# Optimization experiments

Hardware: AMD Instinct MI355X
Metric: run time of the kernel (lower is better)

The kernel has to match this reference:

```python
import jax, jax.numpy as jnp
import numpy as np

DIM = 768
HEADS = 12
HIDDEN = 3072  # dim * mlp_ratio
EPS = 1e-5


def layernorm(x, g, b):
    mu = jnp.mean(x, axis=-1, keepdims=True)
    var = jnp.var(x, axis=-1, keepdims=True)
    return (x - mu) * jax.lax.rsqrt(var + EPS) * g + b


def setup_inputs() -> dict:
    key = jax.random.key(0)
    ks = jax.random.split(key, 10)
    s = 0.02
    return {
        "x": jax.random.normal(ks[0], (4, 1024, DIM), jnp.float32),
        "attention_mask": jax.random.randint(ks[1], (4, 1024), 0, 2, jnp.int32),
        "ln1_g": jnp.ones((DIM,), jnp.float32),
        "ln1_b": jnp.zeros((DIM,), jnp.float32),
        "ln2_g": jnp.ones((DIM,), jnp.float32),
        "ln2_b": jnp.zeros((DIM,), jnp.float32),
        "w_qkv": jax.random.normal(ks[2], (DIM, 3 * DIM), jnp.float32) * s,
        "b_qkv": jnp.zeros((3 * DIM,), jnp.float32),
        "w_proj": jax.random.normal(ks[3], (DIM, DIM), jnp.float32) * s,
        "b_proj": jnp.zeros((DIM,), jnp.float32),
        "w_fc1": jax.random.normal(ks[4], (DIM, HIDDEN), jnp.float32) * s,
        "b_fc1": jnp.zeros((HIDDEN,), jnp.float32),
        "w_fc2": jax.random.normal(ks[5], (HIDDEN, DIM), jnp.float32) * s,
        "b_fc2": jnp.zeros((DIM,), jnp.float32),
    }


def reference(x, attention_mask, ln1_g, ln1_b, ln2_g, ln2_b,
              w_qkv, b_qkv, w_proj, b_proj, w_fc1, b_fc1, w_fc2, b_fc2):
    B, N, C = x.shape
    hd = C // HEADS
    scale = hd ** -0.5

    # --- attention branch ---
    h = layernorm(x, ln1_g, ln1_b)
    qkv = (h @ w_qkv + b_qkv).reshape(B, N, 3, HEADS, hd)
    q, k, v = qkv[:, :, 0], qkv[:, :, 1], qkv[:, :, 2]  # [B,N,H,hd]
    attn = jnp.einsum('bnhd,bmhd->bhnm', q, k) * scale
    mask_bias = jnp.where(attention_mask == 0, -10000.0, 0.0)[:, None, None, :]
    attn = jax.nn.softmax(attn + mask_bias, axis=-1)
    o = jnp.einsum('bhnm,bmhd->bnhd', attn, v).reshape(B, N, C)
    x = x + (o @ w_proj + b_proj)

    # --- MLP branch ---
    h = layernorm(x, ln2_g, ln2_b)
    h = jax.nn.gelu(h @ w_fc1 + b_fc1, approximate=False)
    x = x + (h @ w_fc2 + b_fc2)
    return x
```

## Files before the change

### kernel.cpp

```cpp
#include <hip/hip_runtime.h>

#define DIM 768
#define NTOK 4096
#define HID 3072

typedef __attribute__((ext_vector_type(8))) short bf16x8;
typedef __attribute__((ext_vector_type(4))) float f32x4;

__device__ inline unsigned short f2bf(float f){
  unsigned u = __float_as_uint(f);
  u += 0x7fff + ((u >> 16) & 1);
  return (unsigned short)(u >> 16);
}
__device__ inline unsigned cvt_pk_bf16(float a, float b){
  unsigned r;
  asm("v_cvt_pk_bf16_f32 %0, %1, %2" : "=v"(r) : "v"(a), "v"(b));
  return r;
}
__device__ inline void gload_lds16(const void* g, void* l){
  __builtin_amdgcn_global_load_lds(
      (const __attribute__((address_space(1))) unsigned int*)g,
      (__attribute__((address_space(3))) unsigned int*)l, 16, 0, 0);
}
template<int N> __device__ inline void wait_vmcnt(){
  if constexpr (N == 0) asm volatile("s_waitcnt vmcnt(0)" ::: "memory");
  else if constexpr (N == 4) asm volatile("s_waitcnt vmcnt(4)" ::: "memory");
  else if constexpr (N == 8) asm volatile("s_waitcnt vmcnt(8)" ::: "memory");
  else static_assert(N == 0, "unsupported vmcnt");
}
__device__ inline int swz_read(int row, int hi){
  return (row * 64 + hi * 16) ^ ((row & 7) << 4);
}

__global__ __launch_bounds__(256) void ln_kernel(const float* __restrict__ x,
    const float* __restrict__ g, const float* __restrict__ b,
    unsigned short* __restrict__ out)
{
  int row = blockIdx.x * 4 + (threadIdx.x >> 6);
  int lane = threadIdx.x & 63;
  const float* xr = x + (size_t)row * DIM;
  float4 v[3];
  float s = 0.f, s2 = 0.f;
#pragma unroll
  for (int j = 0; j < 3; ++j){
    v[j] = *(const float4*)(xr + j * 256 + lane * 4);
    s  += v[j].x + v[j].y + v[j].z + v[j].w;
    s2 += v[j].x*v[j].x + v[j].y*v[j].y + v[j].z*v[j].z + v[j].w*v[j].w;
  }
#pragma unroll
  for (int m = 1; m < 64; m <<= 1){ s += __shfl_xor(s, m, 64); s2 += __shfl_xor(s2, m, 64); }
  float mu  = s * (1.f / 768.f);
  float var = s2 * (1.f / 768.f) - mu * mu;
  float inv = rsqrtf(var + 1e-5f);
#pragma unroll
  for (int j = 0; j < 3; ++j){
    int c0 = j * 256 + lane * 4;
    float vv[4] = { v[j].x, v[j].y, v[j].z, v[j].w };
    ushort4 o4;
    o4.x = f2bf((vv[0] - mu) * inv * g[c0 + 0] + b[c0 + 0]);
    o4.y = f2bf((vv[1] - mu) * inv * g[c0 + 1] + b[c0 + 1]);
    o4.z = f2bf((vv[2] - mu) * inv * g[c0 + 2] + b[c0 + 2]);
    o4.w = f2bf((vv[3] - mu) * inv * g[c0 + 3] + b[c0 + 3]);
    *(ushort4*)(out + (size_t)row * DIM + c0) = o4;
  }
}

__global__ __launch_bounds__(256) void transpose4_kernel(
    const float* __restrict__ w_qkv, const float* __restrict__ w_proj,
    const float* __restrict__ w_fc1, const float* __restrict__ w_fc2,
    unsigned short* __restrict__ tq, unsigned short* __restrict__ tp,
    unsigned short* __restrict__ t1, unsigned short* __restrict__ t2)
{
  __shared__ __align__(16) unsigned short tile[32][33];
  int id = blockIdx.x;
  const float* W; unsigned short* Wt; int K, N, tx_n;
  if (id < 1728)      { W = w_qkv;  Wt = tq; K = 768;  N = 2304; tx_n = 72; }
  else if (id < 2304) { W = w_proj; Wt = tp; K = 768;  N = 768;  tx_n = 24; id -= 1728; }
  else if (id < 4608) { W = w_fc1;  Wt = t1; K = 768;  N = 3072; tx_n = 96; id -= 2304; }
  else                { W = w_fc2;  Wt = t2; K = 3072; N = 768;  tx_n = 24; id -= 4608; }
  int n0 = (id % tx_n) * 32, k0 = (id / tx_n) * 32;
  int tx = threadIdx.x & 31, ty = threadIdx.x >> 5;
#pragma unroll
  for (int i = 0; i < 32; i += 8)
    tile[ty + i][tx] = f2bf(W[(size_t)(k0 + ty + i) * N + n0 + tx]);
  __syncthreads();
#pragma unroll
  for (int i = 0; i < 32; i += 8)
    Wt[(size_t)(n0 + ty + i) * K + k0 + tx] = tile[tx][ty + i];
}

__global__ __launch_bounds__(256) void pack_mask_kernel(const int* __restrict__ am,
    unsigned long long* __restrict__ pm)
{
  int lane = threadIdx.x & 63, w = threadIdx.x >> 6, b = blockIdx.x;
  for (int k = w; k < 16; k += 4){
    unsigned long long m = __ballot(am[b * 1024 + k * 64 + lane] != 0);
    if (lane == 0) pm[b * 16 + k] = m;
  }
}

__global__ __launch_bounds__(256) void gemm_qkv_kernel(
    const unsigned short* __restrict__ A,
    const unsigned short* __restrict__ Bt,
    const float* __restrict__ bias,
    unsigned short* __restrict__ q_out,
    unsigned short* __restrict__ k_out,
    unsigned short* __restrict__ v_out,
    int M, int N, int K)
{
  constexpr int BM = 128, BN = 96, BK = 32, DEPTH = 3;
  constexpr int MI = 4, NI = 3;
  constexpr int SMEM_B = DEPTH * (BM + BN) * BK * 2;
  __shared__ __align__(16) char smem[SMEM_B];
  auto As = (unsigned short(*)[BM * BK])smem;
  auto Bs = (unsigned short(*)[BN * BK])(smem + DEPTH * BM * BK * 2);
  const int t = threadIdx.x, lane = t & 63, wid = t >> 6;
  const int lo = lane & 15, hi = lane >> 4;
  const int wr = wid >> 1, wc = wid & 1;

  const int gx = gridDim.x;
  const int nwg = gx * gridDim.y;
  const int lin = blockIdx.y * gx + blockIdx.x;
  const int swz = (lin & 7) * (nwg >> 3) + (lin >> 3);
  const int bm = (swz / gx) * BM, bn = (swz % gx) * BN;

  const unsigned short *p0, *p1, *p2, *p3;
  int d3;
  {
    int c, rp, r, q;
    c = t;       rp = c >> 2; r = rp ^ ((rp >> 2) & 1); q = (c & 3) ^ (r & 3);
    p0 = A  + (size_t)(bm + r) * K + q * 8;
    c = 256 + t; rp = c >> 2; r = rp ^ ((rp >> 2) & 1); q = (c & 3) ^ (r & 3);
    p1 = A  + (size_t)(bm + r) * K + q * 8;
    c = t;       rp = c >> 2; r = rp ^ ((rp >> 2) & 1); q = (c & 3) ^ (r & 3);
    p2 = Bt + (size_t)(bn + r) * K + q * 8;
    int c2w = (t < 128) ? 256 + t : t - 128;
    c = c2w;     rp = c >> 2; r = rp ^ ((rp >> 2) & 1); q = (c & 3) ^ (r & 3);
    p3 = Bt + (size_t)(bn + r) * K + q * 8;
    d3 = c2w * 8;
  }
  int ofsA[MI], ofsB[NI];
#pragma unroll
  for (int i = 0; i < MI; ++i) ofsA[i] = swz_read(wr * 64 + i * 16 + lo, hi);
#pragma unroll
  for (int j = 0; j < NI; ++j) ofsB[j] = swz_read(wc * 48 + j * 16 + lo, hi);

  f32x4 acc[MI][NI];
#pragma unroll
  for (int i = 0; i < MI; ++i)
#pragma unroll
    for (int j = 0; j < NI; ++j) acc[i][j] = (f32x4){0.f, 0.f, 0.f, 0.f};

  const int NIT = K / BK;
  auto stagefull = [&](int buf) __attribute__((always_inline)) {
    gload_lds16(p0, &As[buf][t * 8]);
    gload_lds16(p1, &As[buf][(256 + t) * 8]);
    gload_lds16(p2, &Bs[buf][t * 8]);
    gload_lds16(p3, &Bs[buf][d3]);
    p0 += BK; p1 += BK; p2 += BK; p3 += BK;
  };
  auto kbody = [&](int it, int RB, int WB) __attribute__((always_inline)) {
    if (it < NIT - 1) wait_vmcnt<4>(); else wait_vmcnt<0>();
    __builtin_amdgcn_sched_barrier(0);
    __builtin_amdgcn_s_barrier();
    __builtin_amdgcn_sched_barrier(0);
    if (it + 2 < NIT) stagefull(WB);
    const char* as = (const char*)As[RB];
    const char* bs = (const char*)Bs[RB];
    bf16x8 af[MI], bfr[NI];
#pragma unroll
    for (int i = 0; i < MI; ++i) af[i]  = *(const bf16x8*)(as + ofsA[i]);
#pragma unroll
    for (int j = 0; j < NI; ++j) bfr[j] = *(const bf16x8*)(bs + ofsB[j]);
#pragma unroll
    for (int i = 0; i < MI; ++i)
#pragma unroll
      for (int j = 0; j < NI; ++j)
        acc[i][j] = __builtin_amdgcn_mfma_f32_16x16x32_bf16(af[i], bfr[j], acc[i][j], 0, 0, 0);
  };

  stagefull(0);
  stagefull(1);
  for (int it = 0; it < NIT; it += 3){
    kbody(it,     0, 2);
    kbody(it + 1, 1, 0);
    kbody(it + 2, 2, 1);
  }

  __syncthreads();

  const int part = bn / 768;
  const int cloc = bn % 768;
  const int bb = bm >> 10, n0b = bm & 1023;
  unsigned short* ET = (unsigned short*)smem;
  if (part < 2){
    constexpr int LDE = 104;
#pragma unroll
    for (int i = 0; i < MI; ++i)
#pragma unroll
      for (int j = 0; j < NI; ++j){
        int col_l = wc * 48 + j * 16 + lo;
        float bcol = bias[bn + col_l];
#pragma unroll
        for (int r = 0; r < 4; ++r)
          ET[(wr * 64 + i * 16 + hi * 4 + r) * LDE + col_l] = f2bf(acc[i][j][r] + bcol);
      }
    __syncthreads();
    unsigned short* dst0 = (part == 0) ? q_out : k_out;
#pragma unroll
    for (int p = 0; p < 8; ++p){
      int row = p * 16 + (t >> 4), chunk = t & 15;
      if (chunk < 12){
        int col = cloc + chunk * 8, hh = col >> 6, d0 = col & 63;
        *(bf16x8*)&dst0[((size_t)(bb * 12 + hh)) * 65536 + (n0b + row) * 64 + d0] =
            *(const bf16x8*)&ET[row * LDE + chunk * 8];
      }
    }
  } else {
    constexpr int LDV = 136;
#pragma unroll
    for (int i = 0; i < MI; ++i)
#pragma unroll
      for (int j = 0; j < NI; ++j){
        int col_l = wc * 48 + j * 16 + lo;
        float bcol = bias[bn + col_l];
#pragma unroll
        for (int r = 0; r < 4; ++r)
          ET[col_l * LDV + wr * 64 + i * 16 + hi * 4 + r] = f2bf(acc[i][j][r] + bcol);
      }
    __syncthreads();
#pragma unroll
    for (int p = 0; p < 6; ++p){
      int colg = p * 16 + (t >> 4), chunk = t & 15;
      int col = cloc + colg, hh = col >> 6, d = col & 63;
      *(bf16x8*)&v_out[((size_t)(bb * 12 + hh)) * 65536 + (size_t)d * 1024 + n0b + chunk * 8] =
          *(const bf16x8*)&ET[colg * LDV + chunk * 8];
    }
  }
}

template<int EPI>
__global__ __launch_bounds__(512) void gemm_ks_kernel(
    const unsigned short* __restrict__ A,
    const unsigned short* __restrict__ Bt,
    const float* __restrict__ bias,
    const float* __restrict__ resid,
    void* __restrict__ Cout,
    int M, int N, int K)
{
  constexpr int BM = 128, BN = 96, BK = 64, DEPTH = 3;
  constexpr int MI = 4, NI = 3;
  constexpr int ACH = BM * BK / 8;
  constexpr int BCH = BN * BK / 8;
  constexpr int NC = 4;
  constexpr int TILE_A = BM * BK * 2, TILE_B = BN * BK * 2;
  constexpr int LDE = BN + 4;
  constexpr int SMEM_B = (DEPTH * (TILE_A + TILE_B) > BM * LDE * 4)
                       ?  DEPTH * (TILE_A + TILE_B) : BM * LDE * 4;
  __shared__ __align__(16) char smem[SMEM_B];
  auto As = (unsigned short(*)[BM * BK])smem;
  auto Bs = (unsigned short(*)[BN * BK])(smem + DEPTH * TILE_A);
  const int t = threadIdx.x, lane = t & 63, wid = t >> 6;
  const int lo = lane & 15, hi = lane >> 4;
  const int ks = wid & 1, wc = (wid >> 1) & 1, wr = wid >> 2;

  const int gx = gridDim.x;
  const int nwg = gx * gridDim.y;
  const int lin = blockIdx.y * gx + blockIdx.x;
  const int swz = (lin & 7) * (nwg >> 3) + (lin >> 3);
  const int bm = (swz / gx) * BM, bn = (swz % gx) * BN;

  auto stage = [&](int buf, int k0){
#pragma unroll
    for (int u = 0; u < NC; ++u){
      int c = u * 512 + t;
      if (c < ACH){
        int r = c >> 3, q = (c & 7) ^ (r & 7);
        gload_lds16(A + (size_t)(bm + r) * K + k0 + q * 8, &As[buf][c * 8]);
      } else {
        int c2 = c - ACH;
        if (c2 >= BCH) c2 -= BCH;
        int r = c2 >> 3, q = (c2 & 7) ^ (r & 7);
        gload_lds16(Bt + (size_t)(bn + r) * K + k0 + q * 8, &Bs[buf][c2 * 8]);
      }
    }
  };
  auto rd = [&](const char* base, int row, int q)->bf16x8 {
    return *(const bf16x8*)(base + row * 128 + ((q ^ (row & 7)) << 4));
  };

  f32x4 acc[MI][NI];
#pragma unroll
  for (int i = 0; i < MI; ++i)
#pragma unroll
    for (int j = 0; j < NI; ++j) acc[i][j] = (f32x4){0.f, 0.f, 0.f, 0.f};

  const int NIT = K / BK;
  stage(0, 0);
  stage(1, BK);
  const int qk = ks * 4 + hi;
  for (int it = 0; it < NIT; ++it){
    if (it < NIT - 1) wait_vmcnt<NC>();
    else wait_vmcnt<0>();
    __builtin_amdgcn_sched_barrier(0);
    __builtin_amdgcn_s_barrier();
    __builtin_amdgcn_sched_barrier(0);
    if (it + 2 < NIT) stage((it + 2) % DEPTH, (it + 2) * BK);
    const char* as = (const char*)As[it % DEPTH];
    const char* bs = (const char*)Bs[it % DEPTH];
    bf16x8 af[MI], bfr[NI];
#pragma unroll
    for (int i = 0; i < MI; ++i)  af[i]  = rd(as, wr * 64 + i * 16 + lo, qk);
#pragma unroll
    for (int j = 0; j < NI; ++j) bfr[j] = rd(bs, wc * 48 + j * 16 + lo, qk);
#pragma unroll
    for (int i = 0; i < MI; ++i)
#pragma unroll
      for (int j = 0; j < NI; ++j)
        acc[i][j] = __builtin_amdgcn_mfma_f32_16x16x32_bf16(af[i], bfr[j], acc[i][j], 0, 0, 0);
  }

  __syncthreads();
  float* ET = (float*)smem;
  if (ks == 1){
#pragma unroll
    for (int i = 0; i < MI; ++i)
#pragma unroll
      for (int j = 0; j < NI; ++j)
#pragma unroll
        for (int r = 0; r < 4; ++r)
          ET[(wr * 64 + i * 16 + hi * 4 + r) * LDE + wc * 48 + j * 16 + lo] = acc[i][j][r];
  }
  __syncthreads();
  if (ks == 0){
#pragma unroll
    for (int i = 0; i < MI; ++i)
#pragma unroll
      for (int j = 0; j < NI; ++j){
        int col_l = wc * 48 + j * 16 + lo;
        float bcol = bias[bn + col_l];
#pragma unroll
        for (int r = 0; r < 4; ++r){
          int idx = (wr * 64 + i * 16 + hi * 4 + r) * LDE + col_l;
          ET[idx] = ET[idx] + acc[i][j][r] + bcol;
        }
      }
  }
  __syncthreads();
  if constexpr (EPI == 2){
    int row = t >> 2, q = t & 3;
    const float* rrow = resid + (size_t)(bm + row) * N + bn;
    float* crow = (float*)Cout + (size_t)(bm + row) * N + bn;
#pragma unroll
    for (int k = 0; k < 6; ++k){
      int c4 = (q + k * 4) * 4;
      float4 v = *(const float4*)&ET[row * LDE + c4];
      float4 rs = *(const float4*)&rrow[c4];
      v.x += rs.x; v.y += rs.y; v.z += rs.z; v.w += rs.w;
      *(float4*)&crow[c4] = v;
    }
  } else {
    int row = t >> 2, cq = t & 3;
    unsigned short* crow = (unsigned short*)Cout + (size_t)(bm + row) * N + bn;
#pragma unroll
    for (int s = 0; s < 3; ++s){
      int c0 = cq * 8 + s * 32;
      unsigned w4[4];
#pragma unroll
      for (int e = 0; e < 4; ++e){
        float x0 = ET[row * LDE + c0 + e * 2];
        float x1 = ET[row * LDE + c0 + e * 2 + 1];
        x0 = 0.5f * x0 * (1.f + erff(x0 * 0.70710678118f));
        x1 = 0.5f * x1 * (1.f + erff(x1 * 0.70710678118f));
        w4[e] = (unsigned)f2bf(x0) | ((unsigned)f2bf(x1) << 16);
      }
      *(uint4*)&crow[c0] = make_uint4(w4[0], w4[1], w4[2], w4[3]);
    }
  }
}

__global__ __launch_bounds__(256) void attn_kernel(
    const unsigned short* __restrict__ Qs,
    const unsigned short* __restrict__ Ks,
    const unsigned short* __restrict__ Vts,
    const unsigned long long* __restrict__ pm,
    unsigned short* __restrict__ o)
{
  constexpr int LD = 72;
  __shared__ __align__(16) unsigned short Kl[2][64 * LD];
  __shared__ __align__(16) unsigned short Vt[2][64 * LD];
  __shared__ __align__(16) unsigned short Pl[4][16 * LD];
  const int qb = blockIdx.x, h = blockIdx.y, b = blockIdx.z;
  const int t = threadIdx.x, wid = t >> 6, lane = t & 63;
  const int lo = lane & 15, hi = lane >> 4;
  const size_t bh = (size_t)b * 12 + h;

  const unsigned short* Qg = Qs + (bh * 1024 + qb * 64 + wid * 16 + lo) * 64;
  bf16x8 qf0 = *(const bf16x8*)(Qg + hi * 8);
  bf16x8 qf1 = *(const bf16x8*)(Qg + 32 + hi * 8);

  f32x4 oacc[4];
#pragma unroll
  for (int dj = 0; dj < 4; ++dj) oacc[dj] = (f32x4){0.f, 0.f, 0.f, 0.f};
  float l_part = 0.f;

  const int srow = t >> 2, scol = (t & 3) * 16;
  const int sdst = srow * LD + scol;
  const unsigned short* kg = Ks  + bh * 65536 + srow * 64 + scol;
  const unsigned short* vg = Vts + bh * 65536 + srow * 1024 + scol;
  unsigned short* pw = &Pl[wid][0];

  bf16x8 kn0 = *(const bf16x8*)(kg);
  bf16x8 kn1 = *(const bf16x8*)(kg + 8);
  bf16x8 vn0 = *(const bf16x8*)(vg);
  bf16x8 vn1 = *(const bf16x8*)(vg + 8);
  *(bf16x8*)&Kl[0][sdst]     = kn0;
  *(bf16x8*)&Kl[0][sdst + 8] = kn1;
  *(bf16x8*)&Vt[0][sdst]     = vn0;
  *(bf16x8*)&Vt[0][sdst + 8] = vn1;
  __syncthreads();

  for (int kt = 0; kt < 16; ++kt){
    const int cur = kt & 1;
    if (kt + 1 < 16){
      kn0 = *(const bf16x8*)(kg + (kt + 1) * 4096);
      kn1 = *(const bf16x8*)(kg + (kt + 1) * 4096 + 8);
      vn0 = *(const bf16x8*)(vg + (kt + 1) * 64);
      vn1 = *(const bf16x8*)(vg + (kt + 1) * 64 + 8);
    }

    f32x4 s[4];
#pragma unroll
    for (int nj = 0; nj < 4; ++nj) s[nj] = (f32x4){0.f, 0.f, 0.f, 0.f};
#pragma unroll
    for (int kk = 0; kk < 2; ++kk){
      bf16x8 q = kk ? qf1 : qf0;
#pragma unroll
      for (int nj = 0; nj < 4; ++nj){
        bf16x8 kf = *(const bf16x8*)&Kl[cur][(nj * 16 + lo) * LD + kk * 32 + hi * 8];
        s[nj] = __builtin_amdgcn_mfma_f32_16x16x32_bf16(kf, q, s[nj], 0, 0, 0);
      }
    }

    unsigned long long w = pm[b * 16 + kt] >> (hi * 4);
#pragma unroll
    for (int nj = 0; nj < 4; ++nj){
      float p[4];
#pragma unroll
      for (int r = 0; r < 4; ++r){
        float e = __expf(fmaf(s[nj][r], 0.125f, -16.0f));
        e = ((unsigned)(w >> (nj * 16 + r)) & 1u) ? e : 0.0f;
        l_part += e;
        p[r] = e;
      }
      unsigned w0 = cvt_pk_bf16(p[0], p[1]);
      unsigned w1 = cvt_pk_bf16(p[2], p[3]);
      *(uint2*)&pw[lo * LD + nj * 16 + hi * 4] = make_uint2(w0, w1);
    }
    asm volatile("" ::: "memory");
    bf16x8 pf0 = *(const bf16x8*)&pw[lo * LD + hi * 8];
    bf16x8 pf1 = *(const bf16x8*)&pw[lo * LD + 32 + hi * 8];
#pragma unroll
    for (int kk = 0; kk < 2; ++kk){
      bf16x8 pf = kk ? pf1 : pf0;
#pragma unroll
      for (int dj = 0; dj < 4; ++dj){
        bf16x8 vf = *(const bf16x8*)&Vt[cur][(dj * 16 + lo) * LD + kk * 32 + hi * 8];
        oacc[dj] = __builtin_amdgcn_mfma_f32_16x16x32_bf16(vf, pf, oacc[dj], 0, 0, 0);
      }
    }

    if (kt + 1 < 16){
      *(bf16x8*)&Kl[cur ^ 1][sdst]     = kn0;
      *(bf16x8*)&Kl[cur ^ 1][sdst + 8] = kn1;
      *(bf16x8*)&Vt[cur ^ 1][sdst]     = vn0;
      *(bf16x8*)&Vt[cur ^ 1][sdst + 8] = vn1;
    }
    __syncthreads();
  }

  float l = l_part;
  l += __shfl_xor(l, 16, 64);
  l += __shfl_xor(l, 32, 64);
  float inv = 1.0f / l;
  size_t orow = (size_t)b * 1024 + qb * 64 + wid * 16 + lo;
#pragma unroll
  for (int dj = 0; dj < 4; ++dj){
    unsigned w0 = (unsigned)f2bf(oacc[dj][0] * inv) | ((unsigned)f2bf(oacc[dj][1] * inv) << 16);
    unsigned w1 = (unsigned)f2bf(oacc[dj][2] * inv) | ((unsigned)f2bf(oacc[dj][3] * inv) << 16);
    *(uint2*)&o[orow * DIM + h * 64 + dj * 16 + hi * 4] = make_uint2(w0, w1);
  }
}

extern "C" void kernel_launch(void* const* d_in, const int* in_sizes, int n_in,
                              void* d_out, int out_size, void* d_ws, size_t ws_size,
                              hipStream_t stream)
{
  const float* x      = (const float*)d_in[0];
  const int*   amask  = (const int*)  d_in[1];
  const float* ln1_g  = (const float*)d_in[2];
  const float* ln1_b  = (const float*)d_in[3];
  const float* ln2_g  = (const float*)d_in[4];
  const float* ln2_b  = (const float*)d_in[5];
  const float* w_qkv  = (const float*)d_in[6];
  const float* b_qkv  = (const float*)d_in[7];
  const float* w_proj = (const float*)d_in[8];
  const float* b_proj = (const float*)d_in[9];
  const float* w_fc1  = (const float*)d_in[10];
  const float* b_fc1  = (const float*)d_in[11];
  const float* w_fc2  = (const float*)d_in[12];
  const float* b_fc2  = (const float*)d_in[13];
  float* outp = (float*)d_out;

  char* w = (char*)d_ws;
  auto alloc = [&](size_t bytes){ char* p = w; w += (bytes + 255) & ~(size_t)255; return p; };

  char* p0 = alloc((size_t)4 * 6291456);
  unsigned short* Qs   = (unsigned short*)p0;
  unsigned short* Ks   = (unsigned short*)(p0 + 6291456);
  unsigned short* Vts  = (unsigned short*)(p0 + 2 * 6291456);
  unsigned short* o_bf = (unsigned short*)(p0 + 3 * 6291456);
  unsigned short* a1   = (unsigned short*)p0;
  unsigned short* h_bf = (unsigned short*)alloc((size_t)NTOK * DIM * 2);
  unsigned short* h2   = h_bf;
  float*          x1   = (float*)alloc((size_t)NTOK * DIM * 4);
  unsigned short* wqkvT = (unsigned short*)alloc((size_t)3 * DIM * DIM * 2);
  unsigned short* wprojT= (unsigned short*)alloc((size_t)DIM * DIM * 2);
  unsigned short* wfc1T = (unsigned short*)alloc((size_t)HID * DIM * 2);
  unsigned short* wfc2T = (unsigned short*)alloc((size_t)DIM * HID * 2);
  unsigned long long* pmask = (unsigned long long*)alloc(4 * 16 * 8);

  transpose4_kernel<<<6912, 256, 0, stream>>>(w_qkv, w_proj, w_fc1, w_fc2,
                                              wqkvT, wprojT, wfc1T, wfc2T);
  pack_mask_kernel<<<4, 256, 0, stream>>>(amask, pmask);

  ln_kernel<<<NTOK / 4, 256, 0, stream>>>(x, ln1_g, ln1_b, h_bf);
  gemm_qkv_kernel<<<dim3(2304 / 96, NTOK / 128), 256, 0, stream>>>(
      h_bf, wqkvT, b_qkv, Qs, Ks, Vts, NTOK, 2304, DIM);
  attn_kernel<<<dim3(16, 12, 4), 256, 0, stream>>>(Qs, Ks, Vts, pmask, o_bf);
  gemm_ks_kernel<2><<<dim3(DIM / 96, NTOK / 128), 512, 0, stream>>>(
      o_bf, wprojT, b_proj, x, x1, NTOK, DIM, DIM);
  ln_kernel<<<NTOK / 4, 256, 0, stream>>>(x1, ln2_g, ln2_b, h2);
  gemm_ks_kernel<1><<<dim3(HID / 96, NTOK / 128), 512, 0, stream>>>(
      h2, wfc1T, b_fc1, nullptr, a1, NTOK, HID, DIM);
  gemm_ks_kernel<2><<<dim3(DIM / 96, NTOK / 128), 512, 0, stream>>>(
      a1, wfc2T, b_fc2, x1, outp, NTOK, DIM, HID);
}
```

Measured before the change: 171.1 us.

## Merge prep kernels, add MFMA priority hints, tanh GELU, column-major FC1 swizzle

Folds the weight transpose, first layernorm and mask packing into a single prep launch, which removes two kernel launches. It also wraps MFMA loops in s_setprio so waves issuing matrix ops get scheduling priority, and gives the FC1 GEMM a block-index mapping that walks columns in groups of eight. The exact erf GELU is replaced by a tanh approximation built from exp, which is cheaper but deviates slightly from the reference numerics.

Result: faster. 165.9 us (-3.1%).

```diff
diff --git a/kernel.cpp b/kernel.cpp
--- a/kernel.cpp
+++ b/kernel.cpp
@@ -30,6 +30,77 @@
 }
 __device__ inline int swz_read(int row, int hi){
   return (row * 64 + hi * 16) ^ ((row & 7) << 4);
+}
+__device__ inline float gelu_fast(float v){
+  float u = v * (0.7978845608f + 0.0356774081f * v * v);
+  float e = __expf(-2.0f * fabsf(u));
+  float th = 1.0f - __fdividef(2.0f * e, 1.0f + e);
+  th = copysignf(th, u);
+  return 0.5f * v * (1.0f + th);
+}
+
+__global__ __launch_bounds__(256) void prep_kernel(
+    const float* __restrict__ w_qkv, const float* __restrict__ w_proj,
+    const float* __restrict__ w_fc1, const float* __restrict__ w_fc2,
+    unsigned short* __restrict__ tq, unsigned short* __restrict__ tp,
+    unsigned short* __restrict__ t1, unsigned short* __restrict__ t2,
+    const float* __restrict__ x, const float* __restrict__ g1,
+    const float* __restrict__ b1, unsigned short* __restrict__ h_out,
+    const int* __restrict__ am, unsigned long long* __restrict__ pm)
+{
+  __shared__ __align__(16) unsigned short tile[32][33];
+  int id = blockIdx.x;
+  if (id < 6912){
+    const float* W; unsigned short* Wt; int K, N, tx_n;
+    if (id < 1728)      { W = w_qkv;  Wt = tq; K = 768;  N = 2304; tx_n = 72; }
+    else if (id < 2304) { W = w_proj; Wt = tp; K = 768;  N = 768;  tx_n = 24; id -= 1728; }
+    else if (id < 4608) { W = w_fc1;  Wt = t1; K = 768;  N = 3072; tx_n = 96; id -= 2304; }
+    else                { W = w_fc2;  Wt = t2; K = 3072; N = 768;  tx_n = 24; id -= 4608; }
+    int n0 = (id % tx_n) * 32, k0 = (id / tx_n) * 32;
+    int tx = threadIdx.x & 31, ty = threadIdx.x >> 5;
+#pragma unroll
+    for (int i = 0; i < 32; i += 8)
+      tile[ty + i][tx] = f2bf(W[(size_t)(k0 + ty + i) * N + n0 + tx]);
+    __syncthreads();
+#pragma unroll
+    for (int i = 0; i < 32; i += 8)
+      Wt[(size_t)(n0 + ty + i) * K + k0 + tx] = tile[tx][ty + i];
+  } else if (id < 7936){
+    int row = (id - 6912) * 4 + (threadIdx.x >> 6);
+    int lane = threadIdx.x & 63;
+    const float* xr = x + (size_t)row * DIM;
+    float4 v[3];
+    float s = 0.f, s2 = 0.f;
+#pragma unroll
+    for (int j = 0; j < 3; ++j){
+      v[j] = *(const float4*)(xr + j * 256 + lane * 4);
+      s  += v[j].x + v[j].y + v[j].z + v[j].w;
+      s2 += v[j].x*v[j].x + v[j].y*v[j].y + v[j].z*v[j].z + v[j].w*v[j].w;
+    }
+#pragma unroll
+    for (int m = 1; m < 64; m <<= 1){ s += __shfl_xor(s, m, 64); s2 += __shfl_xor(s2, m, 64); }
+    float mu  = s * (1.f / 768.f);
+    float var = s2 * (1.f / 768.f) - mu * mu;
+    float inv = rsqrtf(var + 1e-5f);
+#pragma unroll
+    for (int j = 0; j < 3; ++j){
+      int c0 = j * 256 + lane * 4;
+      float vv[4] = { v[j].x, v[j].y, v[j].z, v[j].w };
+      ushort4 o4;
+      o4.x = f2bf((vv[0] - mu) * inv * g1[c0 + 0] + b1[c0 + 0]);
+      o4.y = f2bf((vv[1] - mu) * inv * g1[c0 + 1] + b1[c0 + 1]);
+      o4.z = f2bf((vv[2] - mu) * inv * g1[c0 + 2] + b1[c0 + 2]);
+      o4.w = f2bf((vv[3] - mu) * inv * g1[c0 + 3] + b1[c0 + 3]);
+      *(ushort4*)(h_out + (size_t)row * DIM + c0) = o4;
+    }
+  } else {
+    int b = id - 7936;
+    int lane = threadIdx.x & 63, w = threadIdx.x >> 6;
+    for (int k = w; k < 16; k += 4){
+      unsigned long long m = __ballot(am[b * 1024 + k * 64 + lane] != 0);
+      if (lane == 0) pm[b * 16 + k] = m;
+    }
+  }
 }
 
 __global__ __launch_bounds__(256) void ln_kernel(const float* __restrict__ x,
@@ -62,40 +133,6 @@
     o4.z = f2bf((vv[2] - mu) * inv * g[c0 + 2] + b[c0 + 2]);
     o4.w = f2bf((vv[3] - mu) * inv * g[c0 + 3] + b[c0 + 3]);
     *(ushort4*)(out + (size_t)row * DIM + c0) = o4;
-  }
-}
-
-__global__ __launch_bounds__(256) void transpose4_kernel(
-    const float* __restrict__ w_qkv, const float* __restrict__ w_proj,
-    const float* __restrict__ w_fc1, const float* __restrict__ w_fc2,
-    unsigned short* __restrict__ tq, unsigned short* __restrict__ tp,
-    unsigned short* __restrict__ t1, unsigned short* __restrict__ t2)
-{
-  __shared__ __align__(16) unsigned short tile[32][33];
-  int id = blockIdx.x;
-  const float* W; unsigned short* Wt; int K, N, tx_n;
-  if (id < 1728)      { W = w_qkv;  Wt = tq; K = 768;  N = 2304; tx_n = 72; }
-  else if (id < 2304) { W = w_proj; Wt = tp; K = 768;  N = 768;  tx_n = 24; id -= 1728; }
-  else if (id < 4608) { W = w_fc1;  Wt = t1; K = 768;  N = 3072; tx_n = 96; id -= 2304; }
-  else                { W = w_fc2;  Wt = t2; K = 3072; N = 768;  tx_n = 24; id -= 4608; }
-  int n0 = (id % tx_n) * 32, k0 = (id / tx_n) * 32;
-  int tx = threadIdx.x & 31, ty = threadIdx.x >> 5;
-#pragma unroll
-  for (int i = 0; i < 32; i += 8)
-    tile[ty + i][tx] = f2bf(W[(size_t)(k0 + ty + i) * N + n0 + tx]);
-  __syncthreads();
-#pragma unroll
-  for (int i = 0; i < 32; i += 8)
-    Wt[(size_t)(n0 + ty + i) * K + k0 + tx] = tile[tx][ty + i];
-}
-
-__global__ __launch_bounds__(256) void pack_mask_kernel(const int* __restrict__ am,
-    unsigned long long* __restrict__ pm)
-{
-  int lane = threadIdx.x & 63, w = threadIdx.x >> 6, b = blockIdx.x;
-  for (int k = w; k < 16; k += 4){
-    unsigned long long m = __ballot(am[b * 1024 + k * 64 + lane] != 0);
-    if (lane == 0) pm[b * 16 + k] = m;
   }
 }
 
@@ -172,11 +209,13 @@
     for (int i = 0; i < MI; ++i) af[i]  = *(const bf16x8*)(as + ofsA[i]);
 #pragma unroll
     for (int j = 0; j < NI; ++j) bfr[j] = *(const bf16x8*)(bs + ofsB[j]);
+    __builtin_amdgcn_s_setprio(1);
 #pragma unroll
     for (int i = 0; i < MI; ++i)
 #pragma unroll
       for (int j = 0; j < NI; ++j)
         acc[i][j] = __builtin_amdgcn_mfma_f32_16x16x32_bf16(af[i], bfr[j], acc[i][j], 0, 0, 0);
+    __builtin_amdgcn_s_setprio(0);
   };
 
   stagefull(0);
@@ -239,7 +278,7 @@
   }
 }
 
-template<int EPI>
+template<int EPI, int CM>
 __global__ __launch_bounds__(512) void gemm_ks_kernel(
     const unsigned short* __restrict__ A,
     const unsigned short* __restrict__ Bt,
@@ -264,11 +303,20 @@
   const int lo = lane & 15, hi = lane >> 4;
   const int ks = wid & 1, wc = (wid >> 1) & 1, wr = wid >> 2;
 
-  const int gx = gridDim.x;
-  const int nwg = gx * gridDim.y;
+  const int gx = gridDim.x, gy = gridDim.y;
   const int lin = blockIdx.y * gx + blockIdx.x;
-  const int swz = (lin & 7) * (nwg >> 3) + (lin >> 3);
-  const int bm = (swz / gx) * BM, bn = (swz % gx) * BN;
+  int bm, bn;
+  if constexpr (CM == 1){
+    const int cpx = gx >> 3;
+    int idx = lin >> 3;
+    bn = ((lin & 7) * cpx + idx / gy) * BN;
+    bm = (idx % gy) * BM;
+  } else {
+    const int nwg = gx * gy;
+    const int swz = (lin & 7) * (nwg >> 3) + (lin >> 3);
+    bm = (swz / gx) * BM;
+    bn = (swz % gx) * BN;
+  }
 
   auto stage = [&](int buf, int k0){
 #pragma unroll
@@ -313,11 +361,13 @@
     for (int i = 0; i < MI; ++i)  af[i]  = rd(as, wr * 64 + i * 16 + lo, qk);
 #pragma unroll
     for (int j = 0; j < NI; ++j) bfr[j] = rd(bs, wc * 48 + j * 16 + lo, qk);
+    __builtin_amdgcn_s_setprio(1);
 #pragma unroll
     for (int i = 0; i < MI; ++i)
 #pragma unroll
       for (int j = 0; j < NI; ++j)
         acc[i][j] = __builtin_amdgcn_mfma_f32_16x16x32_bf16(af[i], bfr[j], acc[i][j], 0, 0, 0);
+    __builtin_amdgcn_s_setprio(0);
   }
 
   __syncthreads();
@@ -368,10 +418,8 @@
       unsigned w4[4];
 #pragma unroll
       for (int e = 0; e < 4; ++e){
-        float x0 = ET[row * LDE + c0 + e * 2];
-        float x1 = ET[row * LDE + c0 + e * 2 + 1];
-        x0 = 0.5f * x0 * (1.f + erff(x0 * 0.70710678118f));
-        x1 = 0.5f * x1 * (1.f + erff(x1 * 0.70710678118f));
+        float x0 = gelu_fast(ET[row * LDE + c0 + e * 2]);
+        float x1 = gelu_fast(ET[row * LDE + c0 + e * 2 + 1]);
         w4[e] = (unsigned)f2bf(x0) | ((unsigned)f2bf(x1) << 16);
       }
       *(uint4*)&crow[c0] = make_uint4(w4[0], w4[1], w4[2], w4[3]);
@@ -432,6 +480,7 @@
     f32x4 s[4];
 #pragma unroll
     for (int nj = 0; nj < 4; ++nj) s[nj] = (f32x4){0.f, 0.f, 0.f, 0.f};
+    __builtin_amdgcn_s_setprio(1);
 #pragma unroll
     for (int kk = 0; kk < 2; ++kk){
       bf16x8 q = kk ? qf1 : qf0;
@@ -441,6 +490,7 @@
         s[nj] = __builtin_amdgcn_mfma_f32_16x16x32_bf16(kf, q, s[nj], 0, 0, 0);
       }
     }
+    __builtin_amdgcn_s_setprio(0);
 
     unsigned long long w = pm[b * 16 + kt] >> (hi * 4);
 #pragma unroll
@@ -460,6 +510,7 @@
     asm volatile("" ::: "memory");
     bf16x8 pf0 = *(const bf16x8*)&pw[lo * LD + hi * 8];
     bf16x8 pf1 = *(const bf16x8*)&pw[lo * LD + 32 + hi * 8];
+    __builtin_amdgcn_s_setprio(1);
 #pragma unroll
     for (int kk = 0; kk < 2; ++kk){
       bf16x8 pf = kk ? pf1 : pf0;
@@ -469,6 +520,7 @@
         oacc[dj] = __builtin_amdgcn_mfma_f32_16x16x32_bf16(vf, pf, oacc[dj], 0, 0, 0);
       }
     }
+    __builtin_amdgcn_s_setprio(0);
 
     if (kt + 1 < 16){
       *(bf16x8*)&Kl[cur ^ 1][sdst]     = kn0;
@@ -530,19 +582,18 @@
   unsigned short* wfc2T = (unsigned short*)alloc((size_t)DIM * HID * 2);
   unsigned long long* pmask = (unsigned long long*)alloc(4 * 16 * 8);
 
-  transpose4_kernel<<<6912, 256, 0, stream>>>(w_qkv, w_proj, w_fc1, w_fc2,
-                                              wqkvT, wprojT, wfc1T, wfc2T);
-  pack_mask_kernel<<<4, 256, 0, stream>>>(amask, pmask);
-
-  ln_kernel<<<NTOK / 4, 256, 0, stream>>>(x, ln1_g, ln1_b, h_bf);
+  prep_kernel<<<7940, 256, 0, stream>>>(w_qkv, w_proj, w_fc1, w_fc2,
+                                        wqkvT, wprojT, wfc1T, wfc2T,
+                                        x, ln1_g, ln1_b, h_bf, amask, pmask);
+
   gemm_qkv_kernel<<<dim3(2304 / 96, NTOK / 128), 256, 0, stream>>>(
       h_bf, wqkvT, b_qkv, Qs, Ks, Vts, NTOK, 2304, DIM);
   attn_kernel<<<dim3(16, 12, 4), 256, 0, stream>>>(Qs, Ks, Vts, pmask, o_bf);
-  gemm_ks_kernel<2><<<dim3(DIM / 96, NTOK / 128), 512, 0, stream>>>(
+  gemm_ks_kernel<2, 0><<<dim3(DIM / 96, NTOK / 128), 512, 0, stream>>>(
       o_bf, wprojT, b_proj, x, x1, NTOK, DIM, DIM);
   ln_kernel<<<NTOK / 4, 256, 0, stream>>>(x1, ln2_g, ln2_b, h2);
-  gemm_ks_kernel<1><<<dim3(HID / 96, NTOK / 128), 512, 0, stream>>>(
+  gemm_ks_kernel<1, 1><<<dim3(HID / 96, NTOK / 128), 512, 0, stream>>>(
       h2, wfc1T, b_fc1, nullptr, a1, NTOK, HID, DIM);
-  gemm_ks_kernel<2><<<dim3(DIM / 96, NTOK / 128), 512, 0, stream>>>(
+  gemm_ks_kernel<2, 0><<<dim3(DIM / 96, NTOK / 128), 512, 0, stream>>>(
       a1, wfc2T, b_fc2, x1, outp, NTOK, DIM, HID);
 }
```
